# Performance work log

Measured on AMD Instinct MI355X. Metric: run time of the kernel, lower is better.

Reference implementation:

```python
import jax, jax.numpy as jnp
import numpy as np

DIM = 1024
D_STATE = 16
D_CONV = 4
EXPAND = 2
D_INNER = DIM * EXPAND
DT_RANK = 64  # ceil(1024/16)
N_EXP = 8
TOP_K = 2
HID = DIM * 2
B, T = 2, 2048
EPS = 1e-5


def setup_inputs() -> dict:
    key = jax.random.key(0)
    ks = jax.random.split(key, 16)
    s = 0.02
    # dt bias init (softplus-inverse of dt in [1e-3, 1e-1]) as in the torch code
    dt_init = jnp.exp(jax.random.uniform(ks[0], (D_INNER,)) * (np.log(0.1) - np.log(0.001)) + np.log(0.001))
    dt_proj_b = dt_init + jnp.log(-jnp.expm1(-dt_init))
    A_log = jnp.broadcast_to(jnp.log(jnp.arange(1, D_STATE + 1, dtype=jnp.float32))[None, :], (D_INNER, D_STATE))
    return {
        "x": jax.random.normal(ks[1], (B, T, DIM), jnp.float32),
        "ssm_state": jnp.zeros((B, D_INNER, D_STATE), jnp.float32),
        "conv_state": jnp.zeros((B, D_INNER, D_CONV - 1), jnp.float32),
        "ln1_s": jnp.ones((DIM,), jnp.float32), "ln1_b": jnp.zeros((DIM,), jnp.float32),
        "ln2_s": jnp.ones((DIM,), jnp.float32), "ln2_b": jnp.zeros((DIM,), jnp.float32),
        "in_proj_w": jax.random.normal(ks[2], (2 * D_INNER, DIM), jnp.float32) * s,
        "conv_w": jax.random.normal(ks[3], (D_INNER, 1, D_CONV), jnp.float32) * 0.2,
        "conv_b": jnp.zeros((D_INNER,), jnp.float32),
        "x_proj_w": jax.random.normal(ks[4], (DT_RANK + 2 * D_STATE, D_INNER), jnp.float32) * s,
        "dt_proj_w": jax.random.normal(ks[5], (D_INNER, DT_RANK), jnp.float32) * s,
        "dt_proj_b": dt_proj_b,
        "A_log": A_log,
        "Dp": jnp.ones((D_INNER,), jnp.float32),
        "out_proj_w": jax.random.normal(ks[6], (DIM, D_INNER), jnp.float32) * s,
        "router_w": jax.random.normal(ks[7], (N_EXP, DIM), jnp.float32) * s,
        "w_gate": jax.random.normal(ks[8], (N_EXP, HID, DIM), jnp.float32) * s,
        "w_up": jax.random.normal(ks[9], (N_EXP, HID, DIM), jnp.float32) * s,
        "w_down": jax.random.normal(ks[10], (N_EXP, DIM, HID), jnp.float32) * s,
    }


def _layernorm(x, scale, bias):
    mu = x.mean(-1, keepdims=True)
    var = ((x - mu) ** 2).mean(-1, keepdims=True)
    return (x - mu) * jax.lax.rsqrt(var + EPS) * scale + bias


def _mamba(xn, ssm_state, conv_state, in_proj_w, conv_w, conv_b, x_proj_w, dt_proj_w, dt_proj_b, A_log, Dp, out_proj_w):
    xz = jnp.einsum("btd,ed->bte", xn, in_proj_w)          # [B,T,2*di]
    x_in, z = xz[..., :D_INNER], xz[..., D_INNER:]
    # causal depthwise conv with running buffer
    xc = jnp.concatenate([conv_state, x_in.transpose(0, 2, 1)], axis=2)  # [B,di,T+dc-1]
    new_conv_state = xc[:, :, -(D_CONV - 1):]
    conv = jax.lax.conv_general_dilated(xc, conv_w, (1,), "VALID",
                                        dimension_numbers=("NCH", "OIH", "NCH"),
                                        feature_group_count=D_INNER)
    conv = conv + conv_b[None, :, None]
    xcs = jax.nn.silu(conv).transpose(0, 2, 1)              # [B,T,di]
    proj = jnp.einsum("bti,pi->btp", xcs, x_proj_w)
    dt_raw = proj[..., :DT_RANK]
    Bp = proj[..., DT_RANK:DT_RANK + D_STATE]
    Cp = proj[..., DT_RANK + D_STATE:]
    dt = jax.nn.softplus(jnp.einsum("btr,ir->bti", dt_raw, dt_proj_w) + dt_proj_b)
    A = -jnp.exp(A_log)                                     # [di,ds]

    def step(h, inp):
        dt_t, B_t, C_t, x_t = inp                           # [B,di],[B,ds],[B,ds],[B,di]
        dA = jnp.exp(dt_t[..., None] * A)                   # [B,di,ds]
        dB = dt_t[..., None] * B_t[:, None, :]
        h = dA * h + dB * x_t[..., None]
        y = jnp.sum(h * C_t[:, None, :], -1) + Dp * x_t
        return h, y

    xs = (dt.transpose(1, 0, 2), Bp.transpose(1, 0, 2), Cp.transpose(1, 0, 2), xcs.transpose(1, 0, 2))
    h, ys = jax.lax.scan(step, ssm_state, xs)
    y = ys.transpose(1, 0, 2) * jax.nn.silu(z)
    out = jnp.einsum("bti,di->btd", y, out_proj_w)
    return out, h, new_conv_state


def _moe(x, router_w, w_gate, w_up, w_down):
    Bb, Tt, D = x.shape
    xf = x.reshape(-1, D)                                   # [N,D]
    probs = jax.nn.softmax(xf @ router_w.T, axis=-1)        # [N,E]
    tw, ti = jax.lax.top_k(probs, TOP_K)
    tw = tw / tw.sum(-1, keepdims=True)
    gate = jax.nn.silu(jnp.einsum("nd,ehd->neh", xf, w_gate))
    up = jnp.einsum("nd,ehd->neh", xf, w_up)
    eo = jnp.einsum("neh,edh->ned", gate * up, w_down)      # [N,E,D]
    sel = jnp.take_along_axis(eo, ti[:, :, None], axis=1)   # [N,K,D]
    out = (tw[..., None] * sel).sum(1)
    return out.reshape(Bb, Tt, D)


def reference(x, ssm_state, conv_state, ln1_s, ln1_b, ln2_s, ln2_b, in_proj_w, conv_w, conv_b,
              x_proj_w, dt_proj_w, dt_proj_b, A_log, Dp, out_proj_w, router_w, w_gate, w_up, w_down):
    mamba_out, h, new_conv = _mamba(_layernorm(x, ln1_s, ln1_b), ssm_state, conv_state,
                                    in_proj_w, conv_w, conv_b, x_proj_w, dt_proj_w, dt_proj_b,
                                    A_log, Dp, out_proj_w)
    x1 = x + mamba_out
    out = x1 + _moe(_layernorm(x1, ln2_s, ln2_b), router_w, w_gate, w_up, w_down)
    return out
```

## Files before the change

kernel.cpp:

```cpp
#include <hip/hip_runtime.h>
#include <hip/hip_bf16.h>
#include <math.h>

#define DIM 1024
#define D_STATE 16
#define D_CONV 4
#define D_INNER 2048
#define DT_RANK 64
#define N_EXP 8
#define TOP_K 2
#define HID 2048
#define BB 2
#define TT 2048
#define NTOK (BB*TT)
#define NSLOT (NTOK*TOP_K)
#define EPS 1e-5f
#define NCHUNK 64
#define CLEN (TT/NCHUNK)
#define XPJ_KS 8
#define XPJ_KLEN (D_INNER/XPJ_KS)

#define OFF_R0   ((size_t)0)
#define OFF_R1   ((size_t)4194304)
#define OFF_R2   ((size_t)8388608)
#define OFF_XZ   ((size_t)10485760)
#define OFF_H    OFF_XZ
#define OFF_WU   ((size_t)18874368)
#define OFF_XCS  ((size_t)27262976)
#define OFF_DTP  ((size_t)35651584)
#define OFF_X1   ((size_t)44040192)
#define OFF_PROJ ((size_t)48234496)
#define OFF_TW   ((size_t)48627712)
#define OFF_INT  ((size_t)48635904)
#define OFF_XPW  ((size_t)48668672)
#define IO_TI    0
#define IO_CNT   8192
#define IO_CUR   8200
#define IO_OFS   8208
#define IO_TOK   8216
#define IO_SLOT  16408

typedef __attribute__((ext_vector_type(4))) float f32x4;
typedef __attribute__((ext_vector_type(8))) __bf16 bf16x8;
typedef __attribute__((ext_vector_type(4))) __bf16 bf16x4;

__device__ __forceinline__ float siluf(float v){ return v / (1.f + expf(-v)); }

__device__ __forceinline__ f32x4 mfma16(bf16x8 a, bf16x8 b, f32x4 c){
    return __builtin_amdgcn_mfma_f32_16x16x32_bf16(a, b, c, 0, 0, 0);
}

__device__ __forceinline__ void gload16(const void* g, void* l){
    __builtin_amdgcn_global_load_lds(
        (const __attribute__((address_space(1))) unsigned int*)g,
        (__attribute__((address_space(3))) unsigned int*)l, 16, 0, 0);
}

__device__ __forceinline__ void cvt_store16(__bf16* dst, f32x4 a0, f32x4 a1, f32x4 a2, f32x4 a3){
    bf16x8 p0, p1;
    #pragma unroll
    for (int j = 0; j < 4; ++j){
        p0[j]   = (__bf16)a0[j];
        p0[j+4] = (__bf16)a1[j];
        p1[j]   = (__bf16)a2[j];
        p1[j+4] = (__bf16)a3[j];
    }
    *(bf16x8*)dst = p0;
    *(bf16x8*)(dst+8) = p1;
}

__global__ __launch_bounds__(256) void cvt_w_kernel(const float* __restrict__ src,
    __bf16* __restrict__ dst, int n4)
{
    int i = blockIdx.x*256 + threadIdx.x;
    int stride = gridDim.x*256;
    for (; i < n4; i += stride){
        f32x4 v = *(const f32x4*)(src + (size_t)i*4);
        bf16x4 o;
        o[0] = (__bf16)v[0]; o[1] = (__bf16)v[1];
        o[2] = (__bf16)v[2]; o[3] = (__bf16)v[3];
        *(bf16x4*)(dst + (size_t)i*4) = o;
    }
}

__global__ __launch_bounds__(256) void cvt_pad_xproj(const float* __restrict__ src,
    __bf16* __restrict__ dst)
{
    int i = blockIdx.x*256 + threadIdx.x;
    int base = i*4;
    int row = base >> 11;
    bf16x4 o;
    if (row < 96){
        f32x4 v = *(const f32x4*)(src + base);
        o[0] = (__bf16)v[0]; o[1] = (__bf16)v[1];
        o[2] = (__bf16)v[2]; o[3] = (__bf16)v[3];
    } else {
        o[0] = (__bf16)0.f; o[1] = (__bf16)0.f;
        o[2] = (__bf16)0.f; o[3] = (__bf16)0.f;
    }
    *(bf16x4*)(dst + base) = o;
}

__global__ __launch_bounds__(256) void ln_kernel(const float* __restrict__ x,
    const float* __restrict__ s, const float* __restrict__ b,
    __bf16* __restrict__ obf)
{
    int t = blockIdx.x;
    const float* xp = x + (size_t)t * DIM;
    float v[4]; float sum = 0.f, sq = 0.f;
    #pragma unroll
    for (int j = 0; j < 4; ++j){
        v[j] = xp[threadIdx.x + 256*j];
        sum += v[j]; sq += v[j]*v[j];
    }
    #pragma unroll
    for (int off = 32; off; off >>= 1){
        sum += __shfl_xor(sum, off, 64);
        sq  += __shfl_xor(sq , off, 64);
    }
    __shared__ float red[4][2];
    int w = threadIdx.x >> 6, lane = threadIdx.x & 63;
    if (lane == 0){ red[w][0] = sum; red[w][1] = sq; }
    __syncthreads();
    sum = red[0][0]+red[1][0]+red[2][0]+red[3][0];
    sq  = red[0][1]+red[1][1]+red[2][1]+red[3][1];
    float mu = sum * (1.f/DIM);
    float var = sq * (1.f/DIM) - mu*mu;
    float r = rsqrtf(var + EPS);
    #pragma unroll
    for (int j = 0; j < 4; ++j){
        int d = threadIdx.x + 256*j;
        obf[(size_t)t*DIM + d] = (__bf16)((v[j]-mu)*r*s[d] + b[d]);
    }
}

__global__ __launch_bounds__(256) void ln2_router_kernel(const float* __restrict__ x,
    const float* __restrict__ s, const float* __restrict__ b,
    const float* __restrict__ rw, __bf16* __restrict__ obf,
    float* __restrict__ tw, int* __restrict__ ti, int* __restrict__ counts)
{
    int t = blockIdx.x;
    const float* xp = x + (size_t)t * DIM;
    float v[4]; float sum = 0.f, sq = 0.f;
    #pragma unroll
    for (int j = 0; j < 4; ++j){
        v[j] = xp[threadIdx.x + 256*j];
        sum += v[j]; sq += v[j]*v[j];
    }
    #pragma unroll
    for (int off = 32; off; off >>= 1){
        sum += __shfl_xor(sum, off, 64);
        sq  += __shfl_xor(sq , off, 64);
    }
    __shared__ float red[4][2];
    __shared__ float red2[4][N_EXP];
    int w = threadIdx.x >> 6, lane = threadIdx.x & 63;
    if (lane == 0){ red[w][0] = sum; red[w][1] = sq; }
    __syncthreads();
    sum = red[0][0]+red[1][0]+red[2][0]+red[3][0];
    sq  = red[0][1]+red[1][1]+red[2][1]+red[3][1];
    float mu = sum * (1.f/DIM);
    float var = sq * (1.f/DIM) - mu*mu;
    float r = rsqrtf(var + EPS);
    float p[N_EXP] = {};
    #pragma unroll
    for (int j = 0; j < 4; ++j){
        int d = threadIdx.x + 256*j;
        float o = (v[j]-mu)*r*s[d] + b[d];
        obf[(size_t)t*DIM + d] = (__bf16)o;
        #pragma unroll
        for (int e = 0; e < N_EXP; ++e) p[e] += o * rw[e*DIM + d];
    }
    #pragma unroll
    for (int e = 0; e < N_EXP; ++e){
        #pragma unroll
        for (int off = 32; off; off >>= 1) p[e] += __shfl_xor(p[e], off, 64);
    }
    if (lane == 0){
        #pragma unroll
        for (int e = 0; e < N_EXP; ++e) red2[w][e] = p[e];
    }
    __syncthreads();
    if (threadIdx.x == 0){
        float q[N_EXP];
        #pragma unroll
        for (int e = 0; e < N_EXP; ++e)
            q[e] = red2[0][e]+red2[1][e]+red2[2][e]+red2[3][e];
        float mx = q[0];
        #pragma unroll
        for (int e = 1; e < N_EXP; ++e) mx = fmaxf(mx, q[e]);
        float ssum = 0.f;
        #pragma unroll
        for (int e = 0; e < N_EXP; ++e){ q[e] = expf(q[e]-mx); ssum += q[e]; }
        int i0 = 0;
        #pragma unroll
        for (int e = 1; e < N_EXP; ++e) if (q[e] > q[i0]) i0 = e;
        int i1 = (i0 == 0) ? 1 : 0;
        #pragma unroll
        for (int e = 0; e < N_EXP; ++e) if (e != i0 && q[e] > q[i1]) i1 = e;
        float w0 = q[i0]/ssum, w1 = q[i1]/ssum;
        float sw = w0 + w1; w0 /= sw; w1 /= sw;
        tw[t*2] = w0; tw[t*2+1] = w1;
        ti[t*2] = i0; ti[t*2+1] = i1;
        atomicAdd(&counts[i0], 1);
        atomicAdd(&counts[i1], 1);
    }
}

template<int MODE, int EPI, int CBF, int SWZ>
__global__ __launch_bounds__(256,3) void mfma_gemm_fast(
    const __bf16* __restrict__ A, const __bf16* __restrict__ W,
    const void* __restrict__ RG, void* __restrict__ Cv,
    const int* __restrict__ tok_of_slot, const int* __restrict__ counts,
    const int* __restrict__ offs, int M, int N, int K, int lda)
{
    int bx = blockIdx.x, by = blockIdx.y;
    if (SWZ){
        int nwg = gridDim.x*gridDim.y;
        int id = by*gridDim.x + bx;
        int swz = (id & 7)*(nwg >> 3) + (id >> 3);
        bx = swz % gridDim.x; by = swz / gridDim.x;
    }
    int e    = (MODE == 0) ? 0 : blockIdx.z;
    int cnt  = (MODE == 0) ? M : counts[e];
    int base = (MODE == 0) ? 0 : offs[e];
    int m0 = by * 128;
    if (m0 >= cnt) return;
    int n0 = bx * 128;
    const __bf16* We = W + (size_t)e * N * K;

    __shared__ __bf16 As[128*32];
    __shared__ __bf16 Ws[128*32];

    int tid = threadIdx.x;
    int wave = tid >> 6, lane = tid & 63;
    int c0 = wave*2, c1 = wave*2 + 1;
    int lr0 = c0*16 + (lane >> 2);
    int lr1 = c1*16 + (lane >> 2);
    int koff = (lane & 3) * 8;

    int ar0, ar1;
    {
        int m0c = m0 + lr0, m1c = m0 + lr1;
        if (MODE != 0){
            if (m0c >= cnt) m0c = cnt - 1;
            if (m1c >= cnt) m1c = cnt - 1;
        }
        if (MODE == 1){ ar0 = tok_of_slot[base + m0c]; ar1 = tok_of_slot[base + m1c]; }
        else if (MODE == 2){ ar0 = base + m0c; ar1 = base + m1c; }
        else { ar0 = m0c; ar1 = m1c; }
    }
    const __bf16* aS0 = A + (size_t)ar0 * lda + koff;
    const __bf16* aS1 = A + (size_t)ar1 * lda + koff;
    const __bf16* wS0 = We + (size_t)(n0 + lr0) * K + koff;
    const __bf16* wS1 = We + (size_t)(n0 + lr1) * K + koff;
    __bf16* ldsA0 = As + c0*512;
    __bf16* ldsA1 = As + c1*512;
    __bf16* ldsW0 = Ws + c0*512;
    __bf16* ldsW1 = Ws + c1*512;

    int wm = (wave >> 1) * 64, wn = (wave & 1) * 64;
    int fr = lane & 15, fk = (lane >> 4) * 8;

    f32x4 acc[4][4];
    #pragma unroll
    for (int i = 0; i < 4; ++i)
        #pragma unroll
        for (int j = 0; j < 4; ++j)
            acc[i][j] = (f32x4){0.f, 0.f, 0.f, 0.f};

    for (int k0 = 0; k0 < K; k0 += 32){
        gload16(aS0 + k0, ldsA0);
        gload16(aS1 + k0, ldsA1);
        gload16(wS0 + k0, ldsW0);
        gload16(wS1 + k0, ldsW1);
        __syncthreads();
        bf16x8 af[4], bf[4];
        #pragma unroll
        for (int i = 0; i < 4; ++i)
            af[i] = *(const bf16x8*)&As[(wm + i*16 + fr)*32 + fk];
        #pragma unroll
        for (int j = 0; j < 4; ++j)
            bf[j] = *(const bf16x8*)&Ws[(wn + j*16 + fr)*32 + fk];
        #pragma unroll
        for (int i = 0; i < 4; ++i)
            #pragma unroll
            for (int j = 0; j < 4; ++j)
                acc[i][j] = mfma16(af[i], bf[j], acc[i][j]);
        __syncthreads();
    }

    int orow = (lane >> 4) * 4;
    int ocol = lane & 15;
    #pragma unroll
    for (int i = 0; i < 4; ++i){
        #pragma unroll
        for (int jj = 0; jj < 4; ++jj){
            #pragma unroll
            for (int j = 0; j < 4; ++j){
                int m = m0 + wm + i*16 + orow + j;
                int n = n0 + wn + jj*16 + ocol;
                if (m < cnt){
                    size_t row = (size_t)(base + m);
                    float v = acc[i][jj][j];
                    if (EPI == 1) v += ((const float*)RG)[row * (size_t)N + n];
                    if (CBF) ((__bf16*)Cv)[row * (size_t)N + n] = (__bf16)v;
                    else     ((float* )Cv)[row * (size_t)N + n] = v;
                }
            }
        }
    }
}

__global__ __launch_bounds__(256,2) void moe_gateup_fast(
    const __bf16* __restrict__ A, const __bf16* __restrict__ Wg,
    const __bf16* __restrict__ Wu, const int* __restrict__ tok_of_slot,
    const int* __restrict__ counts, const int* __restrict__ offs,
    __bf16* __restrict__ H)
{
    int e = blockIdx.z;
    int cnt = counts[e];
    int base = offs[e];
    int m0 = blockIdx.y * 128;
    if (m0 >= cnt) return;
    int n0 = blockIdx.x * 128;
    const __bf16* Wge = Wg + (size_t)e * HID * DIM;
    const __bf16* Wue = Wu + (size_t)e * HID * DIM;

    __shared__ __bf16 As[128*32];
    __shared__ __bf16 Gs[128*32];
    __shared__ __bf16 Us[128*32];

    int tid = threadIdx.x;
    int wave = tid >> 6, lane = tid & 63;
    int c0 = wave*2, c1 = wave*2 + 1;
    int lr0 = c0*16 + (lane >> 2);
    int lr1 = c1*16 + (lane >> 2);
    int koff = (lane & 3) * 8;

    int m0c = m0 + lr0, m1c = m0 + lr1;
    if (m0c >= cnt) m0c = cnt - 1;
    if (m1c >= cnt) m1c = cnt - 1;
    int ar0 = tok_of_slot[base + m0c];
    int ar1 = tok_of_slot[base + m1c];

    const __bf16* aS0 = A + (size_t)ar0 * DIM + koff;
    const __bf16* aS1 = A + (size_t)ar1 * DIM + koff;
    const __bf16* gS0 = Wge + (size_t)(n0 + lr0) * DIM + koff;
    const __bf16* gS1 = Wge + (size_t)(n0 + lr1) * DIM + koff;
    const __bf16* uS0 = Wue + (size_t)(n0 + lr0) * DIM + koff;
    const __bf16* uS1 = Wue + (size_t)(n0 + lr1) * DIM + koff;
    __bf16* ldsA0 = As + c0*512;
    __bf16* ldsA1 = As + c1*512;
    __bf16* ldsG0 = Gs + c0*512;
    __bf16* ldsG1 = Gs + c1*512;
    __bf16* ldsU0 = Us + c0*512;
    __bf16* ldsU1 = Us + c1*512;

    int wm = (wave >> 1) * 64, wn = (wave & 1) * 64;
    int fr = lane & 15, fk = (lane >> 4) * 8;

    f32x4 accg[4][4], accu[4][4];
    #pragma unroll
    for (int i = 0; i < 4; ++i)
        #pragma unroll
        for (int j = 0; j < 4; ++j){
            accg[i][j] = (f32x4){0.f, 0.f, 0.f, 0.f};
            accu[i][j] = (f32x4){0.f, 0.f, 0.f, 0.f};
        }

    for (int k0 = 0; k0 < DIM; k0 += 32){
        gload16(aS0 + k0, ldsA0);
        gload16(aS1 + k0, ldsA1);
        gload16(gS0 + k0, ldsG0);
        gload16(gS1 + k0, ldsG1);
        gload16(uS0 + k0, ldsU0);
        gload16(uS1 + k0, ldsU1);
        __syncthreads();
        bf16x8 af[4], gf[4], uf[4];
        #pragma unroll
        for (int i = 0; i < 4; ++i){
            af[i] = *(const bf16x8*)&As[(wm + i*16 + fr)*32 + fk];
            gf[i] = *(const bf16x8*)&Gs[(wn + i*16 + fr)*32 + fk];
            uf[i] = *(const bf16x8*)&Us[(wn + i*16 + fr)*32 + fk];
        }
        #pragma unroll
        for (int i = 0; i < 4; ++i)
            #pragma unroll
            for (int j = 0; j < 4; ++j){
                accg[i][j] = mfma16(af[i], gf[j], accg[i][j]);
                accu[i][j] = mfma16(af[i], uf[j], accu[i][j]);
            }
        __syncthreads();
    }

    int orow = (lane >> 4) * 4;
    int ocol = lane & 15;
    #pragma unroll
    for (int i = 0; i < 4; ++i){
        #pragma unroll
        for (int jj = 0; jj < 4; ++jj){
            #pragma unroll
            for (int j = 0; j < 4; ++j){
                int m = m0 + wm + i*16 + orow + j;
                if (m < cnt){
                    int n = n0 + wn + jj*16 + ocol;
                    size_t row = (size_t)(base + m);
                    float g = accg[i][jj][j], u = accu[i][jj][j];
                    H[row * (size_t)HID + n] = (__bf16)(siluf(g) * u);
                }
            }
        }
    }
}

__global__ __launch_bounds__(256,3) void xproj_ks_kernel(
    const __bf16* __restrict__ A, const __bf16* __restrict__ W,
    float* __restrict__ Cpart)
{
    int m0 = blockIdx.y * 128;
    int kbeg = blockIdx.z * XPJ_KLEN;

    __shared__ __bf16 As[128*32];
    __shared__ __bf16 Ws[128*32];

    int tid = threadIdx.x;
    int wave = tid >> 6, lane = tid & 63;
    int c0 = wave*2, c1 = wave*2 + 1;
    int lr0 = c0*16 + (lane >> 2);
    int lr1 = c1*16 + (lane >> 2);
    int koff = (lane & 3) * 8;

    const __bf16* aS0 = A + (size_t)(m0 + lr0) * D_INNER + kbeg + koff;
    const __bf16* aS1 = A + (size_t)(m0 + lr1) * D_INNER + kbeg + koff;
    const __bf16* wS0 = W + (size_t)lr0 * D_INNER + kbeg + koff;
    const __bf16* wS1 = W + (size_t)lr1 * D_INNER + kbeg + koff;
    __bf16* ldsA0 = As + c0*512;
    __bf16* ldsA1 = As + c1*512;
    __bf16* ldsW0 = Ws + c0*512;
    __bf16* ldsW1 = Ws + c1*512;

    int wm = (wave >> 1) * 64, wn = (wave & 1) * 64;
    int fr = lane & 15, fk = (lane >> 4) * 8;

    f32x4 acc[4][4];
    #pragma unroll
    for (int i = 0; i < 4; ++i)
        #pragma unroll
        for (int j = 0; j < 4; ++j)
            acc[i][j] = (f32x4){0.f, 0.f, 0.f, 0.f};

    for (int k0 = 0; k0 < XPJ_KLEN; k0 += 32){
        gload16(aS0 + k0, ldsA0);
        gload16(aS1 + k0, ldsA1);
        gload16(wS0 + k0, ldsW0);
        gload16(wS1 + k0, ldsW1);
        __syncthreads();
        bf16x8 af[4], bf[4];
        #pragma unroll
        for (int i = 0; i < 4; ++i)
            af[i] = *(const bf16x8*)&As[(wm + i*16 + fr)*32 + fk];
        #pragma unroll
        for (int j = 0; j < 4; ++j)
            bf[j] = *(const bf16x8*)&Ws[(wn + j*16 + fr)*32 + fk];
        #pragma unroll
        for (int i = 0; i < 4; ++i)
            #pragma unroll
            for (int j = 0; j < 4; ++j)
                acc[i][j] = mfma16(af[i], bf[j], acc[i][j]);
        __syncthreads();
    }

    float* Cz = Cpart + (size_t)blockIdx.z * NTOK * 128;
    int orow = (lane >> 4) * 4;
    int ocol = lane & 15;
    #pragma unroll
    for (int i = 0; i < 4; ++i){
        #pragma unroll
        for (int jj = 0; jj < 4; ++jj){
            #pragma unroll
            for (int j = 0; j < 4; ++j){
                int m = m0 + wm + i*16 + orow + j;
                int n = wn + jj*16 + ocol;
                Cz[(size_t)m * 128 + n] = acc[i][jj][j];
            }
        }
    }
}

__global__ __launch_bounds__(256) void xproj_reduce(const float* __restrict__ Cpart,
    float* __restrict__ proj)
{
    int idx = blockIdx.x*256 + threadIdx.x;
    int t = idx / 96, n = idx - t*96;
    float s = 0.f;
    #pragma unroll
    for (int z = 0; z < XPJ_KS; ++z)
        s += Cpart[(size_t)z * NTOK * 128 + (size_t)t * 128 + n];
    proj[idx] = s;
}

__global__ __launch_bounds__(256,2) void dt_gemm(
    const float* __restrict__ A, const float* __restrict__ W,
    const float* __restrict__ bias, float* __restrict__ C,
    int M, int N, int K, int lda)
{
    int m0 = blockIdx.y * 128;
    int n0 = blockIdx.x * 128;

    __shared__ __bf16 As[128*32];
    __shared__ __bf16 Ws[128*32];

    int tid = threadIdx.x;
    int srow = tid >> 1;
    int scol = (tid & 1) * 16;

    const float* af = A + (size_t)(m0 + srow) * lda + scol;
    const float* wptr = W + (size_t)(n0 + srow) * K + scol;

    f32x4 raf[4], rw[4];
    #pragma unroll
    for (int q = 0; q < 4; ++q){
        raf[q] = *(const f32x4*)(af + q*4);
        rw[q]  = *(const f32x4*)(wptr + q*4);
    }

    int wave = tid >> 6, lane = tid & 63;
    int wm = (wave >> 1) * 64, wn = (wave & 1) * 64;
    int fr = lane & 15, fk = (lane >> 4) * 8;

    f32x4 acc[4][4];
    #pragma unroll
    for (int i = 0; i < 4; ++i)
        #pragma unroll
        for (int j = 0; j < 4; ++j)
            acc[i][j] = (f32x4){0.f, 0.f, 0.f, 0.f};

    for (int k0 = 0; k0 < K; k0 += 32){
        cvt_store16(&As[srow*32 + scol], raf[0], raf[1], raf[2], raf[3]);
        cvt_store16(&Ws[srow*32 + scol], rw[0], rw[1], rw[2], rw[3]);
        __syncthreads();
        if (k0 + 32 < K){
            #pragma unroll
            for (int q = 0; q < 4; ++q){
                raf[q] = *(const f32x4*)(af + k0 + 32 + q*4);
                rw[q]  = *(const f32x4*)(wptr + k0 + 32 + q*4);
            }
        }
        bf16x8 afr[4], bfr[4];
        #pragma unroll
        for (int i = 0; i < 4; ++i)
            afr[i] = *(const bf16x8*)&As[(wm + i*16 + fr)*32 + fk];
        #pragma unroll
        for (int i = 0; i < 4; ++i)
            bfr[i] = *(const bf16x8*)&Ws[(wn + i*16 + fr)*32 + fk];
        #pragma unroll
        for (int i = 0; i < 4; ++i)
            #pragma unroll
            for (int j = 0; j < 4; ++j)
                acc[i][j] = mfma16(afr[i], bfr[j], acc[i][j]);
        __syncthreads();
    }

    int orow = (lane >> 4) * 4;
    int ocol = lane & 15;
    #pragma unroll
    for (int i = 0; i < 4; ++i){
        #pragma unroll
        for (int jj = 0; jj < 4; ++jj){
            #pragma unroll
            for (int j = 0; j < 4; ++j){
                int m = m0 + wm + i*16 + orow + j;
                int n = n0 + wn + jj*16 + ocol;
                if (m < M && n < N){
                    float v = acc[i][jj][j] + bias[n];
                    v = (v > 20.f) ? v : log1pf(expf(v));
                    C[(size_t)m * N + n] = v;
                }
            }
        }
    }
}

__global__ __launch_bounds__(256) void conv_kernel(const float* __restrict__ xz,
    const float* __restrict__ cs, const float* __restrict__ cw,
    const float* __restrict__ cb, float* __restrict__ xcs,
    __bf16* __restrict__ xcs_bf)
{
    int idx = blockIdx.x*256 + threadIdx.x;
    int d = idx & (D_INNER-1);
    int bt = idx >> 11;
    int b = bt >> 11;
    int t = bt & (TT-1);
    float acc = cb[d];
    #pragma unroll
    for (int k = 0; k < 4; ++k){
        int tau = t + k - 3;
        float xv;
        if (tau >= 0) xv = xz[(size_t)(b*TT + tau)*(2*D_INNER) + d];
        else          xv = cs[((size_t)b*D_INNER + d)*3 + (tau + 3)];
        acc += cw[d*4 + k] * xv;
    }
    float v = siluf(acc);
    xcs[idx] = v;
    xcs_bf[idx] = (__bf16)v;
}

__global__ __launch_bounds__(256) void scan_pass1(const float* __restrict__ dtp,
    const float* __restrict__ proj, const float* __restrict__ xcs,
    const float* __restrict__ A_log, float* __restrict__ hend,
    float* __restrict__ sumdt)
{
    int gid = blockIdx.x*256 + threadIdx.x;
    int bd = gid & (BB*D_INNER-1);
    int chunk = gid >> 12;
    int b = bd >> 11, d = bd & (D_INNER-1);
    float As[D_STATE], h[D_STATE];
    #pragma unroll
    for (int s = 0; s < D_STATE; ++s){
        As[s] = -__expf(A_log[d*D_STATE + s]);
        h[s] = 0.f;
    }
    float sdt = 0.f;
    int base = b*TT + chunk*CLEN;
    for (int t = 0; t < CLEN; ++t){
        size_t bt = (size_t)(base + t);
        float dt = dtp[bt*D_INNER + d];
        float x  = xcs[bt*D_INNER + d];
        f32x4 Bv[4];
        #pragma unroll
        for (int q = 0; q < 4; ++q) Bv[q] = *(const f32x4*)(proj + bt*96 + DT_RANK + q*4);
        float dtx = dt * x;
        sdt += dt;
        #pragma unroll
        for (int s = 0; s < D_STATE; ++s)
            h[s] = __expf(dt*As[s])*h[s] + Bv[s>>2][s&3]*dtx;
    }
    size_t hb = ((size_t)bd*NCHUNK + chunk)*D_STATE;
    #pragma unroll
    for (int q = 0; q < 4; ++q)
        *(f32x4*)(hend + hb + q*4) = (f32x4){h[q*4], h[q*4+1], h[q*4+2], h[q*4+3]};
    sumdt[bd*NCHUNK + chunk] = sdt;
}

__global__ __launch_bounds__(256) void scan_combine(const float* __restrict__ hend,
    const float* __restrict__ sumdt, const float* __restrict__ A_log,
    const float* __restrict__ ssm0, float* __restrict__ hstart)
{
    int gid = blockIdx.x*256 + threadIdx.x;
    int s = gid & 15;
    int bd = gid >> 4;
    int b = bd >> 11, d = bd & (D_INNER-1);
    float As = -__expf(A_log[d*D_STATE + s]);
    float h = ssm0[((size_t)b*D_INNER + d)*D_STATE + s];
    for (int c = 0; c < NCHUNK; ++c){
        size_t idx = ((size_t)bd*NCHUNK + c)*D_STATE + s;
        hstart[idx] = h;
        h = hend[idx] + __expf(As * sumdt[bd*NCHUNK + c]) * h;
    }
}

__global__ __launch_bounds__(256) void scan_pass3(const float* __restrict__ dtp,
    const float* __restrict__ proj, const float* __restrict__ xcs,
    const float* __restrict__ xz, const float* __restrict__ A_log,
    const float* __restrict__ Dp, const float* __restrict__ hstart,
    __bf16* __restrict__ ym)
{
    int gid = blockIdx.x*256 + threadIdx.x;
    int bd = gid & (BB*D_INNER-1);
    int chunk = gid >> 12;
    int b = bd >> 11, d = bd & (D_INNER-1);
    float As[D_STATE], h[D_STATE];
    #pragma unroll
    for (int s = 0; s < D_STATE; ++s)
        As[s] = -__expf(A_log[d*D_STATE + s]);
    size_t hb = ((size_t)bd*NCHUNK + chunk)*D_STATE;
    #pragma unroll
    for (int q = 0; q < 4; ++q){
        f32x4 hv = *(const f32x4*)(hstart + hb + q*4);
        h[q*4] = hv[0]; h[q*4+1] = hv[1]; h[q*4+2] = hv[2]; h[q*4+3] = hv[3];
    }
    float Dd = Dp[d];
    int base = b*TT + chunk*CLEN;
    for (int t = 0; t < CLEN; ++t){
        size_t bt = (size_t)(base + t);
        float dt = dtp[bt*D_INNER + d];
        float x  = xcs[bt*D_INNER + d];
        f32x4 Bv[4], Cv[4];
        #pragma unroll
        for (int q = 0; q < 4; ++q){
            Bv[q] = *(const f32x4*)(proj + bt*96 + DT_RANK + q*4);
            Cv[q] = *(const f32x4*)(proj + bt*96 + DT_RANK + D_STATE + q*4);
        }
        float dtx = dt * x;
        float p = 0.f;
        #pragma unroll
        for (int s = 0; s < D_STATE; ++s){
            h[s] = __expf(dt*As[s])*h[s] + Bv[s>>2][s&3]*dtx;
            p += h[s] * Cv[s>>2][s&3];
        }
        float y = p + Dd*x;
        float z = xz[bt*(2*D_INNER) + D_INNER + d];
        float sz = z / (1.f + __expf(-z));
        ym[bt*D_INNER + d] = (__bf16)(y * sz);
    }
}

__global__ void offs_kernel(const int* __restrict__ counts, int* __restrict__ offs)
{
    if (threadIdx.x == 0 && blockIdx.x == 0){
        int s = 0;
        for (int e = 0; e < N_EXP; ++e){ offs[e] = s; s += counts[e]; }
    }
}

__global__ __launch_bounds__(256) void assign_kernel(const int* __restrict__ ti,
    const int* __restrict__ offs, int* __restrict__ cursors,
    int* __restrict__ tok_of_slot, int* __restrict__ slot_of)
{
    int t = blockIdx.x*256 + threadIdx.x;
    if (t >= NTOK) return;
    #pragma unroll
    for (int k = 0; k < TOP_K; ++k){
        int e = ti[t*2 + k];
        int pos = atomicAdd(&cursors[e], 1);
        int slot = offs[e] + pos;
        tok_of_slot[slot] = t;
        slot_of[t*2 + k] = slot;
    }
}

__global__ __launch_bounds__(256) void final_kernel(const float* __restrict__ x1,
    const float* __restrict__ down_out, const float* __restrict__ tw,
    const int* __restrict__ slot_of, float* __restrict__ out)
{
    int idx4 = blockIdx.x*256 + threadIdx.x;
    int t = idx4 >> 8;
    int c = idx4 & 255;
    float w0 = tw[t*2], w1 = tw[t*2+1];
    size_t s0 = (size_t)slot_of[t*2] * DIM;
    size_t s1 = (size_t)slot_of[t*2+1] * DIM;
    float4 a = *(const float4*)(x1 + (size_t)t*DIM + c*4);
    float4 d0 = *(const float4*)(down_out + s0 + c*4);
    float4 d1 = *(const float4*)(down_out + s1 + c*4);
    float4 r;
    r.x = a.x + w0*d0.x + w1*d1.x;
    r.y = a.y + w0*d0.y + w1*d1.y;
    r.z = a.z + w0*d0.z + w1*d1.z;
    r.w = a.w + w0*d0.w + w1*d1.w;
    *(float4*)(out + (size_t)t*DIM + c*4) = r;
}

extern "C" void kernel_launch(void* const* d_in, const int* in_sizes, int n_in,
                              void* d_out, int out_size, void* d_ws, size_t ws_size,
                              hipStream_t stream)
{
    const float* x        = (const float*)d_in[0];
    const float* ssm0     = (const float*)d_in[1];
    const float* conv0    = (const float*)d_in[2];
    const float* ln1_s    = (const float*)d_in[3];
    const float* ln1_b    = (const float*)d_in[4];
    const float* ln2_s    = (const float*)d_in[5];
    const float* ln2_b    = (const float*)d_in[6];
    const float* in_proj  = (const float*)d_in[7];
    const float* conv_w   = (const float*)d_in[8];
    const float* conv_b   = (const float*)d_in[9];
    const float* x_proj   = (const float*)d_in[10];
    const float* dt_proj  = (const float*)d_in[11];
    const float* dt_b     = (const float*)d_in[12];
    const float* A_log    = (const float*)d_in[13];
    const float* Dp       = (const float*)d_in[14];
    const float* out_proj = (const float*)d_in[15];
    const float* router_w = (const float*)d_in[16];
    const float* w_gate   = (const float*)d_in[17];
    const float* w_up     = (const float*)d_in[18];
    const float* w_down   = (const float*)d_in[19];
    float* out = (float*)d_out;

    float* ws = (float*)d_ws;
    __bf16* xn_bf  = (__bf16*)(ws + OFF_R0);
    float*  hend   = ws + OFF_R0;
    __bf16* ym_bf  = (__bf16*)(ws + OFF_R0);
    float*  xpart  = ws + OFF_R1;
    float*  hst    = ws + OFF_R1;
    float*  sdt    = ws + OFF_R2;
    __bf16* opbf   = (__bf16*)(ws + OFF_R2);
    __bf16* xn2bf  = (__bf16*)(ws + OFF_R2);
    float*  xz     = ws + OFF_XZ;
    __bf16* H      = (__bf16*)(ws + OFF_H);
    __bf16* wubf   = (__bf16*)(ws + OFF_WU);
    float*  xcs    = ws + OFF_XCS;
    float*  dnout  = ws + OFF_XCS;
    float*  dtp    = ws + OFF_DTP;
    __bf16* ipbf   = (__bf16*)(ws + OFF_DTP);
    __bf16* wgbf   = (__bf16*)(ws + OFF_DTP);
    __bf16* wdbf   = (__bf16*)(ws + OFF_DTP);
    __bf16* xcs_bf = (__bf16*)(ws + OFF_X1);
    float*  x1     = ws + OFF_X1;
    float*  proj   = ws + OFF_PROJ;
    float*  tw     = ws + OFF_TW;
    __bf16* xpw    = (__bf16*)(ws + OFF_XPW);
    int*    ip     = (int*)(ws + OFF_INT);
    int* ti          = ip + IO_TI;
    int* counts      = ip + IO_CNT;
    int* cursors     = ip + IO_CUR;
    int* offs        = ip + IO_OFS;
    int* tok_of_slot = ip + IO_TOK;
    int* slot_of     = ip + IO_SLOT;

    hipMemsetAsync(counts, 0, 16*sizeof(int), stream);

    cvt_w_kernel<<<1024, 256, 0, stream>>>(in_proj, ipbf, (2*D_INNER*DIM)/4);
    ln_kernel<<<NTOK, 256, 0, stream>>>(x, ln1_s, ln1_b, xn_bf);
    mfma_gemm_fast<0,0,0,1><<<dim3(32,32), 256, 0, stream>>>(xn_bf, ipbf, nullptr, xz,
        nullptr, nullptr, nullptr, NTOK, 2*D_INNER, DIM, DIM);
    conv_kernel<<<(NTOK*D_INNER)/256, 256, 0, stream>>>(xz, conv0, conv_w, conv_b, xcs, xcs_bf);
    cvt_pad_xproj<<<256, 256, 0, stream>>>(x_proj, xpw);
    xproj_ks_kernel<<<dim3(1,32,XPJ_KS), 256, 0, stream>>>(xcs_bf, xpw, xpart);
    xproj_reduce<<<(NTOK*96)/256, 256, 0, stream>>>(xpart, proj);
    dt_gemm<<<dim3(16,32), 256, 0, stream>>>(proj, dt_proj, dt_b, dtp,
        NTOK, D_INNER, DT_RANK, 96);
    scan_pass1<<<1024, 256, 0, stream>>>(dtp, proj, xcs, A_log, hend, sdt);
    scan_combine<<<256, 256, 0, stream>>>(hend, sdt, A_log, ssm0, hst);
    scan_pass3<<<1024, 256, 0, stream>>>(dtp, proj, xcs, xz, A_log, Dp, hst, ym_bf);
    cvt_w_kernel<<<512, 256, 0, stream>>>(out_proj, opbf, (DIM*D_INNER)/4);
    mfma_gemm_fast<0,1,0,1><<<dim3(8,32), 256, 0, stream>>>(ym_bf, opbf, x, x1,
        nullptr, nullptr, nullptr, NTOK, DIM, D_INNER, D_INNER);
    ln2_router_kernel<<<NTOK, 256, 0, stream>>>(x1, ln2_s, ln2_b, router_w,
        xn2bf, tw, ti, counts);
    offs_kernel<<<1, 64, 0, stream>>>(counts, offs);
    assign_kernel<<<NTOK/256, 256, 0, stream>>>(ti, offs, cursors, tok_of_slot, slot_of);
    cvt_w_kernel<<<2048, 256, 0, stream>>>(w_gate, wgbf, (N_EXP*HID*DIM)/4);
    cvt_w_kernel<<<2048, 256, 0, stream>>>(w_up, wubf, (N_EXP*HID*DIM)/4);
    moe_gateup_fast<<<dim3(HID/128, 64, N_EXP), 256, 0, stream>>>(xn2bf, wgbf, wubf,
        tok_of_slot, counts, offs, H);
    cvt_w_kernel<<<2048, 256, 0, stream>>>(w_down, wdbf, (N_EXP*DIM*HID)/4);
    mfma_gemm_fast<2,0,0,0><<<dim3(DIM/128, 64, N_EXP), 256, 0, stream>>>(H, wdbf, nullptr, dnout,
        tok_of_slot, counts, offs, NSLOT, DIM, HID, HID);
    final_kernel<<<(NTOK*DIM/4)/256, 256, 0, stream>>>(x1, dnout, tw, slot_of, out);
}
```

Measured before the change: 744.3 us.

## Double-buffer LDS tiles with async prefetch and XOR swizzle in GEMM kernels

```diff
diff --git a/kernel.cpp b/kernel.cpp
--- a/kernel.cpp
+++ b/kernel.cpp
@@ -229,15 +229,15 @@
     int n0 = bx * 128;
     const __bf16* We = W + (size_t)e * N * K;
 
-    __shared__ __bf16 As[128*32];
-    __shared__ __bf16 Ws[128*32];
+    __shared__ __bf16 As[2*128*32];
+    __shared__ __bf16 Ws[2*128*32];
 
     int tid = threadIdx.x;
     int wave = tid >> 6, lane = tid & 63;
     int c0 = wave*2, c1 = wave*2 + 1;
     int lr0 = c0*16 + (lane >> 2);
     int lr1 = c1*16 + (lane >> 2);
-    int koff = (lane & 3) * 8;
+    int koff = (((lane & 3) ^ ((lane >> 3) & 3)) * 8);
 
     int ar0, ar1;
     {
@@ -260,7 +260,8 @@
     __bf16* ldsW1 = Ws + c1*512;
 
     int wm = (wave >> 1) * 64, wn = (wave & 1) * 64;
-    int fr = lane & 15, fk = (lane >> 4) * 8;
+    int fr = lane & 15;
+    const int scb = (((lane >> 4) ^ ((lane >> 1) & 3)) * 8);
 
     f32x4 acc[4][4];
     #pragma unroll
@@ -269,25 +270,38 @@
         for (int j = 0; j < 4; ++j)
             acc[i][j] = (f32x4){0.f, 0.f, 0.f, 0.f};
 
+    gload16(aS0, ldsA0);
+    gload16(aS1, ldsA1);
+    gload16(wS0, ldsW0);
+    gload16(wS1, ldsW1);
+
+    int bo = 0;
     for (int k0 = 0; k0 < K; k0 += 32){
-        gload16(aS0 + k0, ldsA0);
-        gload16(aS1 + k0, ldsA1);
-        gload16(wS0 + k0, ldsW0);
-        gload16(wS1 + k0, ldsW1);
-        __syncthreads();
+        int nbo = bo ^ 4096;
+        if (k0 + 32 < K){
+            gload16(aS0 + k0 + 32, ldsA0 + nbo);
+            gload16(aS1 + k0 + 32, ldsA1 + nbo);
+            gload16(wS0 + k0 + 32, ldsW0 + nbo);
+            gload16(wS1 + k0 + 32, ldsW1 + nbo);
+            asm volatile("s_waitcnt vmcnt(4)" ::: "memory");
+        } else {
+            asm volatile("s_waitcnt vmcnt(0)" ::: "memory");
+        }
+        __builtin_amdgcn_s_barrier();
         bf16x8 af[4], bf[4];
         #pragma unroll
         for (int i = 0; i < 4; ++i)
-            af[i] = *(const bf16x8*)&As[(wm + i*16 + fr)*32 + fk];
+            af[i] = *(const bf16x8*)&As[bo + (wm + i*16 + fr)*32 + scb];
         #pragma unroll
         for (int j = 0; j < 4; ++j)
-            bf[j] = *(const bf16x8*)&Ws[(wn + j*16 + fr)*32 + fk];
+            bf[j] = *(const bf16x8*)&Ws[bo + (wn + j*16 + fr)*32 + scb];
         #pragma unroll
         for (int i = 0; i < 4; ++i)
             #pragma unroll
             for (int j = 0; j < 4; ++j)
                 acc[i][j] = mfma16(af[i], bf[j], acc[i][j]);
-        __syncthreads();
+        __builtin_amdgcn_s_barrier();
+        bo = nbo;
     }
 
     int orow = (lane >> 4) * 4;
@@ -327,16 +341,16 @@
     const __bf16* Wge = Wg + (size_t)e * HID * DIM;
     const __bf16* Wue = Wu + (size_t)e * HID * DIM;
 
-    __shared__ __bf16 As[128*32];
-    __shared__ __bf16 Gs[128*32];
-    __shared__ __bf16 Us[128*32];
+    __shared__ __bf16 As[2*128*32];
+    __shared__ __bf16 Gs[2*128*32];
+    __shared__ __bf16 Us[2*128*32];
 
     int tid = threadIdx.x;
     int wave = tid >> 6, lane = tid & 63;
     int c0 = wave*2, c1 = wave*2 + 1;
     int lr0 = c0*16 + (lane >> 2);
     int lr1 = c1*16 + (lane >> 2);
-    int koff = (lane & 3) * 8;
+    int koff = (((lane & 3) ^ ((lane >> 3) & 3)) * 8);
 
     int m0c = m0 + lr0, m1c = m0 + lr1;
     if (m0c >= cnt) m0c = cnt - 1;
@@ -358,7 +372,8 @@
     __bf16* ldsU1 = Us + c1*512;
 
     int wm = (wave >> 1) * 64, wn = (wave & 1) * 64;
-    int fr = lane & 15, fk = (lane >> 4) * 8;
+    int fr = lane & 15;
+    const int scb = (((lane >> 4) ^ ((lane >> 1) & 3)) * 8);
 
     f32x4 accg[4][4], accu[4][4];
     #pragma unroll
@@ -369,20 +384,34 @@
             accu[i][j] = (f32x4){0.f, 0.f, 0.f, 0.f};
         }
 
+    gload16(aS0, ldsA0);
+    gload16(aS1, ldsA1);
+    gload16(gS0, ldsG0);
+    gload16(gS1, ldsG1);
+    gload16(uS0, ldsU0);
+    gload16(uS1, ldsU1);
+
+    int bo = 0;
     for (int k0 = 0; k0 < DIM; k0 += 32){
-        gload16(aS0 + k0, ldsA0);
-        gload16(aS1 + k0, ldsA1);
-        gload16(gS0 + k0, ldsG0);
-        gload16(gS1 + k0, ldsG1);
-        gload16(uS0 + k0, ldsU0);
-        gload16(uS1 + k0, ldsU1);
-        __syncthreads();
+        int nbo = bo ^ 4096;
+        if (k0 + 32 < DIM){
+            gload16(aS0 + k0 + 32, ldsA0 + nbo);
+            gload16(aS1 + k0 + 32, ldsA1 + nbo);
+            gload16(gS0 + k0 + 32, ldsG0 + nbo);
+            gload16(gS1 + k0 + 32, ldsG1 + nbo);
+            gload16(uS0 + k0 + 32, ldsU0 + nbo);
+            gload16(uS1 + k0 + 32, ldsU1 + nbo);
+            asm volatile("s_waitcnt vmcnt(6)" ::: "memory");
+        } else {
+            asm volatile("s_waitcnt vmcnt(0)" ::: "memory");
+        }
+        __builtin_amdgcn_s_barrier();
         bf16x8 af[4], gf[4], uf[4];
         #pragma unroll
         for (int i = 0; i < 4; ++i){
-            af[i] = *(const bf16x8*)&As[(wm + i*16 + fr)*32 + fk];
-            gf[i] = *(const bf16x8*)&Gs[(wn + i*16 + fr)*32 + fk];
-            uf[i] = *(const bf16x8*)&Us[(wn + i*16 + fr)*32 + fk];
+            af[i] = *(const bf16x8*)&As[bo + (wm + i*16 + fr)*32 + scb];
+            gf[i] = *(const bf16x8*)&Gs[bo + (wn + i*16 + fr)*32 + scb];
+            uf[i] = *(const bf16x8*)&Us[bo + (wn + i*16 + fr)*32 + scb];
         }
         #pragma unroll
         for (int i = 0; i < 4; ++i)
@@ -391,7 +420,8 @@
                 accg[i][j] = mfma16(af[i], gf[j], accg[i][j]);
                 accu[i][j] = mfma16(af[i], uf[j], accu[i][j]);
             }
-        __syncthreads();
+        __builtin_amdgcn_s_barrier();
+        bo = nbo;
     }
 
     int orow = (lane >> 4) * 4;
@@ -421,15 +451,15 @@
     int m0 = blockIdx.y * 128;
     int kbeg = blockIdx.z * XPJ_KLEN;
 
-    __shared__ __bf16 As[128*32];
-    __shared__ __bf16 Ws[128*32];
+    __shared__ __bf16 As[2*128*32];
+    __shared__ __bf16 Ws[2*128*32];
 
     int tid = threadIdx.x;
     int wave = tid >> 6, lane = tid & 63;
     int c0 = wave*2, c1 = wave*2 + 1;
     int lr0 = c0*16 + (lane >> 2);
     int lr1 = c1*16 + (lane >> 2);
-    int koff = (lane & 3) * 8;
+    int koff = (((lane & 3) ^ ((lane >> 3) & 3)) * 8);
 
     const __bf16* aS0 = A + (size_t)(m0 + lr0) * D_INNER + kbeg + koff;
     const __bf16* aS1 = A + (size_t)(m0 + lr1) * D_INNER + kbeg + koff;
@@ -441,7 +471,8 @@
     __bf16* ldsW1 = Ws + c1*512;
 
     int wm = (wave >> 1) * 64, wn = (wave & 1) * 64;
-    int fr = lane & 15, fk = (lane >> 4) * 8;
+    int fr = lane & 15;
+    const int scb = (((lane >> 4) ^ ((lane >> 1) & 3)) * 8);
 
     f32x4 acc[4][4];
     #pragma unroll
@@ -450,25 +481,38 @@
         for (int j = 0; j < 4; ++j)
             acc[i][j] = (f32x4){0.f, 0.f, 0.f, 0.f};
 
+    gload16(aS0, ldsA0);
+    gload16(aS1, ldsA1);
+    gload16(wS0, ldsW0);
+    gload16(wS1, ldsW1);
+
+    int bo = 0;
     for (int k0 = 0; k0 < XPJ_KLEN; k0 += 32){
-        gload16(aS0 + k0, ldsA0);
-        gload16(aS1 + k0, ldsA1);
-        gload16(wS0 + k0, ldsW0);
-        gload16(wS1 + k0, ldsW1);
-        __syncthreads();
+        int nbo = bo ^ 4096;
+        if (k0 + 32 < XPJ_KLEN){
+            gload16(aS0 + k0 + 32, ldsA0 + nbo);
+            gload16(aS1 + k0 + 32, ldsA1 + nbo);
+            gload16(wS0 + k0 + 32, ldsW0 + nbo);
+            gload16(wS1 + k0 + 32, ldsW1 + nbo);
+            asm volatile("s_waitcnt vmcnt(4)" ::: "memory");
+        } else {
+            asm volatile("s_waitcnt vmcnt(0)" ::: "memory");
+        }
+        __builtin_amdgcn_s_barrier();
         bf16x8 af[4], bf[4];
         #pragma unroll
         for (int i = 0; i < 4; ++i)
-            af[i] = *(const bf16x8*)&As[(wm + i*16 + fr)*32 + fk];
+            af[i] = *(const bf16x8*)&As[bo + (wm + i*16 + fr)*32 + scb];
         #pragma unroll
         for (int j = 0; j < 4; ++j)
-            bf[j] = *(const bf16x8*)&Ws[(wn + j*16 + fr)*32 + fk];
+            bf[j] = *(const bf16x8*)&Ws[bo + (wn + j*16 + fr)*32 + scb];
         #pragma unroll
         for (int i = 0; i < 4; ++i)
             #pragma unroll
             for (int j = 0; j < 4; ++j)
                 acc[i][j] = mfma16(af[i], bf[j], acc[i][j]);
-        __syncthreads();
+        __builtin_amdgcn_s_barrier();
+        bo = nbo;
     }
 
     float* Cz = Cpart + (size_t)blockIdx.z * NTOK * 128;
```

Result: no change. 740.0 us (-0.6%).
